# Kernel tuning notes

Hardware: AMD Instinct MI355X
Metric: run time of the kernel (lower is better)

## Reference

```python
import jax, jax.numpy as jnp
from jax import lax
import numpy as np

B, S, D = 64, 512, 256
VOCAB, NC = 50000, 10
N_STEPS = 10  # ode_step=11 points -> 10 intervals, h=0.1
BN_EPS = 1e-5


def setup_inputs() -> dict:
    key = jax.random.key(0)
    ks = jax.random.split(key, 16)
    inp = {}
    inp['input_ids'] = jax.random.randint(ks[0], (B, S), 0, VOCAB)
    inp['emb'] = jax.random.normal(ks[1], (VOCAB, D), dtype=jnp.float32)
    inp['W_ode'] = 0.1 * jax.random.normal(ks[2], (D, D), dtype=jnp.float32)  # init std=0.1
    inp['b_ode'] = jnp.zeros((D,), dtype=jnp.float32)
    for i, kk in enumerate([3, 4, 5]):
        fan_in = D * kk
        inp[f'w{kk}'] = jax.random.normal(ks[3 + 3 * i], (128, D, kk), jnp.float32) / np.sqrt(fan_in)
        inp[f'b{kk}'] = jax.random.normal(ks[4 + 3 * i], (128,), jnp.float32) * 0.01
        inp[f'g{kk}'] = jnp.ones((128,), jnp.float32)
        inp[f'be{kk}'] = jnp.zeros((128,), jnp.float32)
    inp['wc'] = jax.random.normal(ks[12], (NC, D + 3 * 128), jnp.float32) / np.sqrt(D + 3 * 128)
    inp['bc'] = jnp.zeros((NC,), jnp.float32)
    return inp


def _forward(input_ids, emb, W_ode, b_ode, w3, b3, g3, be3, w4, b4, g4, be4,
             w5, b5, g5, be5, wc, bc):
    x = emb[input_ids]                      # (B,S,D)
    # --- Neural ODE branch: linear RHS f(z) = z W^T + b, RK4 fixed-step on [0,1] ---
    z0 = x.reshape(-1, D)                   # (B*S, D)
    h = jnp.float32(1.0 / N_STEPS)

    def f(z):
        return z @ W_ode.T + b_ode

    def step(z, _):
        k1 = f(z)
        k2 = f(z + 0.5 * h * k1)
        k3 = f(z + 0.5 * h * k2)
        k4 = f(z + h * k3)
        return z + (h / 6.0) * (k1 + 2 * k2 + 2 * k3 + k4), None

    z, _ = lax.scan(step, z0, None, length=N_STEPS)
    node_pooled = z.reshape(B, S, D).max(axis=1)   # global max over seq -> (B,D)

    # --- TextCNN branches on raw embeddings ---
    cin = jnp.transpose(x, (0, 2, 1))       # (B,D,S)
    inv_std = jnp.float32(1.0 / np.sqrt(1.0 + BN_EPS))  # BN eval: mean=0, var=1

    def branch(w, b, g, be):
        c = lax.conv_general_dilated(cin, w, (1,), 'VALID',
                                     dimension_numbers=('NCH', 'OIH', 'NCH'))
        c = c + b[None, :, None]
        c = g[None, :, None] * (c * inv_std) + be[None, :, None]
        c = jax.nn.relu(c)
        return c.max(axis=2)                # (B,128)

    p3 = branch(w3, b3, g3, be3)
    p4 = branch(w4, b4, g4, be4)
    p5 = branch(w5, b5, g5, be5)

    feats = jnp.concatenate([node_pooled, p3, p4, p5], axis=1)  # (B,640)
    return feats @ wc.T + bc                # (B,NC); dropout is identity in eval


def reference(input_ids, emb, W_ode, b_ode, w3, b3, g3, be3, w4, b4, g4, be4,
              w5, b5, g5, be5, wc, bc):
    return _forward(input_ids, emb, W_ode, b_ode, w3, b3, g3, be3,
                    w4, b4, g4, be4, w5, b5, g5, be5, wc, bc)
```

## Files before the change

kernel.cpp:

```cpp
#include <hip/hip_runtime.h>


typedef short bf16x8 __attribute__((ext_vector_type(8)));
typedef float f32x4 __attribute__((ext_vector_type(4)));

__device__ __forceinline__ unsigned short f2bf(float f) {
  unsigned u = __float_as_uint(f);
  u += 0x7FFFu + ((u >> 16) & 1u);
  return (unsigned short)(u >> 16);
}

__device__ __forceinline__ float dotcol64(const float* __restrict__ xrow,
                                          const float* __restrict__ Y, int c) {
  float a0 = 0.f, a1 = 0.f, a2 = 0.f, a3 = 0.f;
#pragma unroll 1
  for (int w = 0; w < 4; ++w) {
    float bv[64];
#pragma unroll
    for (int v = 0; v < 64; ++v) bv[v] = Y[(w * 64 + v) * 256 + c];
#pragma unroll
    for (int v = 0; v < 64; v += 4) {
      a0 = fmaf(xrow[w * 64 + v + 0], bv[v + 0], a0);
      a1 = fmaf(xrow[w * 64 + v + 1], bv[v + 1], a1);
      a2 = fmaf(xrow[w * 64 + v + 2], bv[v + 2], a2);
      a3 = fmaf(xrow[w * 64 + v + 3], bv[v + 3], a3);
    }
  }
  return (a0 + a1) + (a2 + a3);
}

__global__ __launch_bounds__(256) void k_prep1(
    const float* __restrict__ W, const float* __restrict__ bode,
    const float* __restrict__ w3c, const float* __restrict__ w4c, const float* __restrict__ w5c,
    float* __restrict__ Bm, float* __restrict__ c1,
    unsigned short* __restrict__ slab, unsigned* __restrict__ featbuf) {
  __shared__ float r1[256], r2[256], r3[256], red[4];
  const int tid = threadIdx.x, blk = blockIdx.x;
  if (blk < 256) {
    const int i = blk;
    r1[tid] = W[i * 256 + tid];
    __syncthreads();
    const float v2 = dotcol64(r1, W, tid);
    r2[tid] = v2;
    __syncthreads();
    const float v3 = dotcol64(r2, W, tid);
    r3[tid] = v3;
    __syncthreads();
    const float v4 = dotcol64(r3, W, tid);
    const float w1 = r1[tid];
    Bm[i * 256 + tid] = 0.1f * w1 + 0.005f * v2
                      + (0.001f / 6.f) * v3 + (0.0001f / 24.f) * v4;
    const float q = 0.05f * w1 + (0.01f / 6.f) * v2 + (0.001f / 24.f) * v3;
    float val = bode[tid] * q;
#pragma unroll
    for (int off = 32; off > 0; off >>= 1) val += __shfl_down(val, off);
    if ((tid & 63) == 0) red[tid >> 6] = val;
    __syncthreads();
    if (tid == 0) c1[i] = 0.1f * (bode[i] + ((red[0] + red[1]) + (red[2] + red[3])));
  } else {
    const int base = (blk - 256) * 256 + tid;
#pragma unroll
    for (int u = 0; u < 4; ++u) {
      int e = base + u * 98304;
      int s = e >> 15, r = e & 32767;
      int o = r >> 8, kd = r & 255;
      const float* w; int k, j;
      if (s < 3)      { w = w3c; k = 3; j = s; }
      else if (s < 7) { w = w4c; k = 4; j = s - 3; }
      else            { w = w5c; k = 5; j = s - 7; }
      float val = w[(o * 256 + kd) * k + j];
      int kc = kd >> 5, quad = (kd >> 3) & 3, q8 = kd & 7;
      slab[s * 32768 + ((kc * 4 + quad) * 128 + o) * 8 + q8] = f2bf(val);
    }
    if (base < 64 * 640) featbuf[base] = 0u;
  }
}

__global__ __launch_bounds__(256) void k_prep2a(
    const float* __restrict__ Bm, const float* __restrict__ c1v,
    float* __restrict__ Dm, float* __restrict__ c1b) {
  __shared__ float r1[256], c1s[256], red[4];
  const int tid = threadIdx.x, i = blockIdx.x;
  r1[tid] = Bm[i * 256 + tid];
  c1s[tid] = c1v[tid];
  __syncthreads();
  const float v2 = dotcol64(r1, Bm, tid);
  Dm[i * 256 + tid] = 2.f * r1[tid] + v2;
  float pd = r1[tid] * c1s[tid];
#pragma unroll
  for (int off = 32; off > 0; off >>= 1) pd += __shfl_down(pd, off);
  if ((tid & 63) == 0) red[tid >> 6] = pd;
  __syncthreads();
  if (tid == 0) c1b[i] = 2.f * c1s[i] + ((red[0] + red[1]) + (red[2] + red[3]));
}

__global__ __launch_bounds__(256) void k_prep2b(
    const float* __restrict__ Dm, const float* __restrict__ c1bv,
    float* __restrict__ c10, unsigned short* __restrict__ slab) {
  __shared__ float curs[256], cbs[256], red[4];
  const int tid = threadIdx.x, i = blockIdx.x;
  const float coefN[6] = {1.f, 5.f, 10.f, 10.f, 5.f, 1.f};
  const float coefC[5] = {5.f, 10.f, 10.f, 5.f, 1.f};
  float v = Dm[i * 256 + tid];
  curs[tid] = v;
  cbs[tid] = c1bv[tid];
  __syncthreads();
  float n10 = ((i == tid) ? 1.f : 0.f) + coefN[1] * v;
  float pd = v * cbs[tid];
#pragma unroll
  for (int off = 32; off > 0; off >>= 1) pd += __shfl_down(pd, off);
  if ((tid & 63) == 0) red[tid >> 6] = pd;
  __syncthreads();
  float ct = coefC[0] * cbs[i] + coefC[1] * ((red[0] + red[1]) + (red[2] + red[3]));

#pragma unroll 1
  for (int k = 2; k <= 5; ++k) {
    v = dotcol64(curs, Dm, tid);
    __syncthreads();
    curs[tid] = v;
    n10 = fmaf(coefN[k], v, n10);
    float pdk = v * cbs[tid];
#pragma unroll
    for (int off = 32; off > 0; off >>= 1) pdk += __shfl_down(pdk, off);
    if ((tid & 63) == 0) red[tid >> 6] = pdk;
    __syncthreads();
    if (k <= 4) ct = fmaf(coefC[k], (red[0] + red[1]) + (red[2] + red[3]), ct);
  }

  {
    const int o = i, kd = tid;
    const int kc = kd >> 5, quad = (kd >> 3) & 3, q8 = kd & 7;
    slab[(12 + (o >> 7)) * 32768 + ((kc * 4 + quad) * 128 + (o & 127)) * 8 + q8] = f2bf(n10);
  }
  if (tid == 0) c10[i] = ct;
}


__global__ __launch_bounds__(256, 2) void k_main(
    const int* __restrict__ ids, const float* __restrict__ emb,
    const unsigned short* __restrict__ slab, const float* __restrict__ ctot,
    const float* __restrict__ b3, const float* __restrict__ g3, const float* __restrict__ be3,
    const float* __restrict__ b4, const float* __restrict__ g4, const float* __restrict__ be4,
    const float* __restrict__ b5, const float* __restrict__ g5, const float* __restrict__ be5,
    unsigned* __restrict__ featbuf) {
  __shared__ alignas(16) unsigned short Xt[68 * 264];
  __shared__ int ids_s[68];
  const int tid = threadIdx.x;
  const int blk = blockIdx.x;
  const int b = blk >> 3;
  const int t0 = (blk & 7) * 64;
  const int lane = tid & 63;
  const int wave = tid >> 6;
  const int m15 = lane & 15;
  const int quad = lane >> 4;

  if (tid < 68) {
    int t = t0 + tid;
    ids_s[tid] = (t < 512) ? ids[b * 512 + t] : -1;
  }
  __syncthreads();

  const unsigned short* fb0 = slab + ((size_t)quad * 128 + wave * 2 * 16 + m15) * 8;
  bf16x8 fA[4], fB[4], fC[4], fD[4];
#define LDFRAG(DST, EN)                                                         \
  {                                                                             \
    const unsigned short* p_ = fb0 + (EN) * 8192;                               \
    DST[0] = *(const bf16x8*)(p_);                                              \
    DST[1] = *(const bf16x8*)(p_ + 128);                                        \
    DST[2] = *(const bf16x8*)(p_ + 4096);                                       \
    DST[3] = *(const bf16x8*)(p_ + 4096 + 128);                                 \
  }
  LDFRAG(fA, 0) LDFRAG(fB, 1) LDFRAG(fC, 2) LDFRAG(fD, 3)

  for (int i = tid; i < 68 * 64; i += 256) {
    int row = i >> 6, s4 = i & 63;
    uint2 v = make_uint2(0u, 0u);
    int id = ids_s[row];
    if (id >= 0) {
      const float4 f = *(const float4*)(emb + (size_t)id * 256 + s4 * 4);
      v.x = (unsigned)f2bf(f.x) | ((unsigned)f2bf(f.y) << 16);
      v.y = (unsigned)f2bf(f.z) | ((unsigned)f2bf(f.w) << 16);
    }
    *(uint2*)&Xt[row * 264 + s4 * 4] = v;
  }
  __syncthreads();

  f32x4 acc[4][2];
#pragma unroll
  for (int mt = 0; mt < 4; ++mt)
#pragma unroll
    for (int nt = 0; nt < 2; ++nt) acc[mt][nt] = (f32x4){0.f, 0.f, 0.f, 0.f};

#define ENTRY(KCQ, FR)                                                          \
  {                                                                             \
    _Pragma("unroll")                                                           \
    for (int kc2 = 0; kc2 < 2; ++kc2) {                                         \
      const int kd0 = ((KCQ) * 2 + kc2) * 32 + quad * 8;                        \
      bf16x8 af[4];                                                             \
      _Pragma("unroll")                                                         \
      for (int mt = 0; mt < 4; ++mt)                                            \
        af[mt] = *(const bf16x8*)&Xt[(shift + mt * 16 + m15) * 264 + kd0];      \
      _Pragma("unroll")                                                         \
      for (int mt = 0; mt < 4; ++mt) {                                          \
        acc[mt][0] = __builtin_amdgcn_mfma_f32_16x16x32_bf16(af[mt], FR[kc2 * 2 + 0], acc[mt][0], 0, 0, 0); \
        acc[mt][1] = __builtin_amdgcn_mfma_f32_16x16x32_bf16(af[mt], FR[kc2 * 2 + 1], acc[mt][1], 0, 0, 0); \
      }                                                                         \
    }                                                                           \
  }

  for (int eq = 0; eq < 14; ++eq) {
    const int shift = (eq < 3) ? eq : (eq < 7) ? (eq - 3) : (eq < 12) ? (eq - 7) : 0;

    ENTRY(0, fA) if (eq < 13) LDFRAG(fA, (eq + 1) * 4 + 0)
    ENTRY(1, fB) if (eq < 13) LDFRAG(fB, (eq + 1) * 4 + 1)
    ENTRY(2, fC) if (eq < 13) LDFRAG(fC, (eq + 1) * 4 + 2)
    ENTRY(3, fD) if (eq < 13) LDFRAG(fD, (eq + 1) * 4 + 3)

    const int g = (eq == 2) ? 0 : (eq == 6) ? 1 : (eq == 11) ? 2
                : (eq == 12) ? 3 : (eq == 13) ? 4 : -1;
    if (g >= 0) {
      if (g < 3) {
        const int kk = g + 3;
        const float* bb  = (g == 0) ? b3 : (g == 1) ? b4 : b5;
        const float* gg  = (g == 0) ? g3 : (g == 1) ? g4 : g5;
        const float* bbe = (g == 0) ? be3 : (g == 1) ? be4 : be5;
        const int off = 256 + g * 128;
        const int tmax = 512 - kk;
#pragma unroll
        for (int nt = 0; nt < 2; ++nt) {
          const int n = (wave * 2 + nt) * 16 + m15;
          const float sc = gg[n] * 0.9999950000375f;
          const float sh = fmaf(sc, bb[n], bbe[n]);
          float mx = 0.f;
#pragma unroll
          for (int mt = 0; mt < 4; ++mt)
#pragma unroll
            for (int r = 0; r < 4; ++r) {
              const int t = t0 + mt * 16 + quad * 4 + r;
              const float v = fmaf(sc, acc[mt][nt][r], sh);
              if (t <= tmax) mx = fmaxf(mx, v);
            }
          mx = fmaxf(mx, __shfl_xor(mx, 16));
          mx = fmaxf(mx, __shfl_xor(mx, 32));
          if (quad == 0) atomicMax(&featbuf[b * 640 + off + n], __float_as_uint(mx));
        }
      } else {
        const int base = (g == 3) ? 0 : 128;
#pragma unroll
        for (int nt = 0; nt < 2; ++nt) {
          const int n = (wave * 2 + nt) * 16 + m15;
          const float ct = ctot[base + n];
          float mx = -3.4e38f;
#pragma unroll
          for (int mt = 0; mt < 4; ++mt)
#pragma unroll
            for (int r = 0; r < 4; ++r)
              mx = fmaxf(mx, acc[mt][nt][r] + ct);
          mx = fmaxf(mx, __shfl_xor(mx, 16));
          mx = fmaxf(mx, __shfl_xor(mx, 32));
          if (quad == 0) {
            unsigned bits = __float_as_uint(mx);
            unsigned key = (bits & 0x80000000u) ? ~bits : (bits | 0x80000000u);
            atomicMax(&featbuf[b * 640 + base + n], key);
          }
        }
      }
#pragma unroll
      for (int mt = 0; mt < 4; ++mt)
#pragma unroll
        for (int nt = 0; nt < 2; ++nt) acc[mt][nt] = (f32x4){0.f, 0.f, 0.f, 0.f};
    }
  }
#undef ENTRY
#undef LDFRAG
}

__global__ void k_fin(const unsigned* __restrict__ featbuf, const float* __restrict__ wc,
                      const float* __restrict__ bc, float* __restrict__ out) {
  int b = blockIdx.x, lane = threadIdx.x;
  float p[10];
#pragma unroll
  for (int c = 0; c < 10; ++c) p[c] = 0.f;
  for (int f = lane; f < 640; f += 64) {
    unsigned u = featbuf[b * 640 + f];
    float v;
    if (f < 256) v = (u & 0x80000000u) ? __uint_as_float(u ^ 0x80000000u) : __uint_as_float(~u);
    else v = __uint_as_float(u);
#pragma unroll
    for (int c = 0; c < 10; ++c) p[c] = fmaf(v, wc[c * 640 + f], p[c]);
  }
#pragma unroll
  for (int c = 0; c < 10; ++c) {
    float s = p[c];
#pragma unroll
    for (int off = 32; off > 0; off >>= 1) s += __shfl_down(s, off);
    if (lane == 0) out[b * 10 + c] = s + bc[c];
  }
}

extern "C" void kernel_launch(void* const* d_in, const int* in_sizes, int n_in,
                              void* d_out, int out_size, void* d_ws, size_t ws_size,
                              hipStream_t stream) {
  (void)in_sizes; (void)n_in; (void)out_size; (void)ws_size;
  const int*   ids  = (const int*)d_in[0];
  const float* emb  = (const float*)d_in[1];
  const float* W    = (const float*)d_in[2];
  const float* bode = (const float*)d_in[3];
  const float* w3   = (const float*)d_in[4];
  const float* b3   = (const float*)d_in[5];
  const float* g3   = (const float*)d_in[6];
  const float* be3  = (const float*)d_in[7];
  const float* w4   = (const float*)d_in[8];
  const float* b4   = (const float*)d_in[9];
  const float* g4   = (const float*)d_in[10];
  const float* be4  = (const float*)d_in[11];
  const float* w5   = (const float*)d_in[12];
  const float* b5   = (const float*)d_in[13];
  const float* g5   = (const float*)d_in[14];
  const float* be5  = (const float*)d_in[15];
  const float* wc   = (const float*)d_in[16];
  const float* bc   = (const float*)d_in[17];
  float* out = (float*)d_out;

  float* wsf = (float*)d_ws;
  float* Bm  = wsf;
  float* Dm  = wsf + 65536;
  float* c1  = wsf + 131072;
  float* c1b = wsf + 131328;
  float* c10 = wsf + 131584;
  unsigned short* slab = (unsigned short*)(wsf + 131840);
  unsigned* featbuf = (unsigned*)(wsf + 361216);

  hipLaunchKernelGGL(k_prep1, dim3(640), dim3(256), 0, stream,
                     W, bode, w3, w4, w5, Bm, c1, slab, featbuf);
  hipLaunchKernelGGL(k_prep2a, dim3(256), dim3(256), 0, stream, Bm, c1, Dm, c1b);
  hipLaunchKernelGGL(k_prep2b, dim3(256), dim3(256), 0, stream, Dm, c1b, c10, slab);
  hipLaunchKernelGGL(k_main, dim3(512), dim3(256), 0, stream,
                     ids, emb, slab, c10,
                     b3, g3, be3, b4, g4, be4, b5, g5, be5, featbuf);
  hipLaunchKernelGGL(k_fin, dim3(64), dim3(64), 0, stream, featbuf, wc, bc, out);
}
```

Before: 195.7 us.

## Halve k_main time tile to 32, double grid, double-buffer weight fragments

Each k_main block now covers 32 sequence positions instead of 64, so the grid grows to 1024 blocks and launch bounds rise to 4 blocks per CU. Weight-fragment prefetch drops from four buffers to two, so the loop now runs 28 steps over two slab entries each. MFMA sections are wrapped in s_setprio. The goal is more occupancy and less register and LDS use per block. The cost is that every slab fragment is re-read by twice as many blocks, with more global and L2 traffic and twice as many atomicMax updates.

```diff
diff --git a/kernel.cpp b/kernel.cpp
--- a/kernel.cpp
+++ b/kernel.cpp
@@ -136,43 +136,30 @@
 }
 
 
-__global__ __launch_bounds__(256, 2) void k_main(
+__global__ __launch_bounds__(256, 4) void k_main(
     const int* __restrict__ ids, const float* __restrict__ emb,
     const unsigned short* __restrict__ slab, const float* __restrict__ ctot,
     const float* __restrict__ b3, const float* __restrict__ g3, const float* __restrict__ be3,
     const float* __restrict__ b4, const float* __restrict__ g4, const float* __restrict__ be4,
     const float* __restrict__ b5, const float* __restrict__ g5, const float* __restrict__ be5,
     unsigned* __restrict__ featbuf) {
-  __shared__ alignas(16) unsigned short Xt[68 * 264];
-  __shared__ int ids_s[68];
+  __shared__ alignas(16) unsigned short Xt[36 * 264];
+  __shared__ int ids_s[36];
   const int tid = threadIdx.x;
   const int blk = blockIdx.x;
-  const int b = blk >> 3;
-  const int t0 = (blk & 7) * 64;
+  const int b = blk & 63;
+  const int t0 = (blk >> 6) * 32;
   const int lane = tid & 63;
   const int wave = tid >> 6;
   const int m15 = lane & 15;
   const int quad = lane >> 4;
 
-  if (tid < 68) {
+  if (tid < 36) {
     int t = t0 + tid;
     ids_s[tid] = (t < 512) ? ids[b * 512 + t] : -1;
   }
   __syncthreads();
-
-  const unsigned short* fb0 = slab + ((size_t)quad * 128 + wave * 2 * 16 + m15) * 8;
-  bf16x8 fA[4], fB[4], fC[4], fD[4];
-#define LDFRAG(DST, EN)                                                         \
-  {                                                                             \
-    const unsigned short* p_ = fb0 + (EN) * 8192;                               \
-    DST[0] = *(const bf16x8*)(p_);                                              \
-    DST[1] = *(const bf16x8*)(p_ + 128);                                        \
-    DST[2] = *(const bf16x8*)(p_ + 4096);                                       \
-    DST[3] = *(const bf16x8*)(p_ + 4096 + 128);                                 \
-  }
-  LDFRAG(fA, 0) LDFRAG(fB, 1) LDFRAG(fC, 2) LDFRAG(fD, 3)
-
-  for (int i = tid; i < 68 * 64; i += 256) {
+  for (int i = tid; i < 36 * 64; i += 256) {
     int row = i >> 6, s4 = i & 63;
     uint2 v = make_uint2(0u, 0u);
     int id = ids_s[row];
@@ -185,39 +172,66 @@
   }
   __syncthreads();
 
-  f32x4 acc[4][2];
-#pragma unroll
-  for (int mt = 0; mt < 4; ++mt)
+  const unsigned short* fb0 = slab + ((size_t)quad * 128 + (wave * 2 + 0) * 16 + m15) * 8;
+  const unsigned short* fb1 = fb0 + 128;
+
+  bf16x8 fA[4], fB[4];
+#pragma unroll
+  for (int q = 0; q < 4; ++q) {
+    fA[q] = *(const bf16x8*)(((q & 1) ? fb1 : fb0) + (q >> 1) * 4096);
+    fB[q] = *(const bf16x8*)(((q & 1) ? fb1 : fb0) + 8192 + (q >> 1) * 4096);
+  }
+
+  f32x4 acc[2][2];
+#pragma unroll
+  for (int mt = 0; mt < 2; ++mt)
 #pragma unroll
     for (int nt = 0; nt < 2; ++nt) acc[mt][nt] = (f32x4){0.f, 0.f, 0.f, 0.f};
 
 #define ENTRY(KCQ, FR)                                                          \
   {                                                                             \
+    __builtin_amdgcn_s_setprio(1);                                              \
     _Pragma("unroll")                                                           \
     for (int kc2 = 0; kc2 < 2; ++kc2) {                                         \
       const int kd0 = ((KCQ) * 2 + kc2) * 32 + quad * 8;                        \
-      bf16x8 af[4];                                                             \
+      bf16x8 af[2];                                                             \
       _Pragma("unroll")                                                         \
-      for (int mt = 0; mt < 4; ++mt)                                            \
+      for (int mt = 0; mt < 2; ++mt)                                            \
         af[mt] = *(const bf16x8*)&Xt[(shift + mt * 16 + m15) * 264 + kd0];      \
       _Pragma("unroll")                                                         \
-      for (int mt = 0; mt < 4; ++mt) {                                          \
+      for (int mt = 0; mt < 2; ++mt) {                                          \
         acc[mt][0] = __builtin_amdgcn_mfma_f32_16x16x32_bf16(af[mt], FR[kc2 * 2 + 0], acc[mt][0], 0, 0, 0); \
         acc[mt][1] = __builtin_amdgcn_mfma_f32_16x16x32_bf16(af[mt], FR[kc2 * 2 + 1], acc[mt][1], 0, 0, 0); \
       }                                                                         \
     }                                                                           \
-  }
-
-  for (int eq = 0; eq < 14; ++eq) {
-    const int shift = (eq < 3) ? eq : (eq < 7) ? (eq - 3) : (eq < 12) ? (eq - 7) : 0;
-
-    ENTRY(0, fA) if (eq < 13) LDFRAG(fA, (eq + 1) * 4 + 0)
-    ENTRY(1, fB) if (eq < 13) LDFRAG(fB, (eq + 1) * 4 + 1)
-    ENTRY(2, fC) if (eq < 13) LDFRAG(fC, (eq + 1) * 4 + 2)
-    ENTRY(3, fD) if (eq < 13) LDFRAG(fD, (eq + 1) * 4 + 3)
-
-    const int g = (eq == 2) ? 0 : (eq == 6) ? 1 : (eq == 11) ? 2
-                : (eq == 12) ? 3 : (eq == 13) ? 4 : -1;
+    __builtin_amdgcn_s_setprio(0);                                              \
+  }
+
+  for (int ep = 0; ep < 28; ++ep) {
+    const int e0 = ep * 2;
+    const int slice = e0 >> 2;
+    const int shift = (slice < 3) ? slice
+                    : (slice < 7) ? (slice - 3)
+                    : (slice < 12) ? (slice - 7) : 0;
+    const int kcq0 = e0 & 3;
+
+    ENTRY(kcq0, fA);
+    if (ep < 27) {
+      const int eo = (e0 + 2) * 8192;
+#pragma unroll
+      for (int q = 0; q < 4; ++q)
+        fA[q] = *(const bf16x8*)(((q & 1) ? fb1 : fb0) + eo + (q >> 1) * 4096);
+    }
+    ENTRY(kcq0 + 1, fB);
+    if (ep < 27) {
+      const int eo = (e0 + 3) * 8192;
+#pragma unroll
+      for (int q = 0; q < 4; ++q)
+        fB[q] = *(const bf16x8*)(((q & 1) ? fb1 : fb0) + eo + (q >> 1) * 4096);
+    }
+
+    const int g = (ep == 5) ? 0 : (ep == 13) ? 1 : (ep == 23) ? 2
+                : (ep == 25) ? 3 : (ep == 27) ? 4 : -1;
     if (g >= 0) {
       if (g < 3) {
         const int kk = g + 3;
@@ -233,7 +247,7 @@
           const float sh = fmaf(sc, bb[n], bbe[n]);
           float mx = 0.f;
 #pragma unroll
-          for (int mt = 0; mt < 4; ++mt)
+          for (int mt = 0; mt < 2; ++mt)
 #pragma unroll
             for (int r = 0; r < 4; ++r) {
               const int t = t0 + mt * 16 + quad * 4 + r;
@@ -252,7 +266,7 @@
           const float ct = ctot[base + n];
           float mx = -3.4e38f;
 #pragma unroll
-          for (int mt = 0; mt < 4; ++mt)
+          for (int mt = 0; mt < 2; ++mt)
 #pragma unroll
             for (int r = 0; r < 4; ++r)
               mx = fmaxf(mx, acc[mt][nt][r] + ct);
@@ -266,13 +280,12 @@
         }
       }
 #pragma unroll
-      for (int mt = 0; mt < 4; ++mt)
+      for (int mt = 0; mt < 2; ++mt)
 #pragma unroll
         for (int nt = 0; nt < 2; ++nt) acc[mt][nt] = (f32x4){0.f, 0.f, 0.f, 0.f};
     }
   }
 #undef ENTRY
-#undef LDFRAG
 }
 
 __global__ void k_fin(const unsigned* __restrict__ featbuf, const float* __restrict__ wc,
@@ -335,7 +348,7 @@
                      W, bode, w3, w4, w5, Bm, c1, slab, featbuf);
   hipLaunchKernelGGL(k_prep2a, dim3(256), dim3(256), 0, stream, Bm, c1, Dm, c1b);
   hipLaunchKernelGGL(k_prep2b, dim3(256), dim3(256), 0, stream, Dm, c1b, c10, slab);
-  hipLaunchKernelGGL(k_main, dim3(512), dim3(256), 0, stream,
+  hipLaunchKernelGGL(k_main, dim3(1024), dim3(256), 0, stream,
                      ids, emb, slab, c10,
                      b3, g3, be3, b4, g4, be4, b5, g5, be5, featbuf);
   hipLaunchKernelGGL(k_fin, dim3(64), dim3(64), 0, stream, featbuf, wc, bc, out);
```

Result: slower. 202.7 us (+3.6%).

## Double block sizes: split-K prep matvecs and 8-wave MFMA tiling in main

Applied to the files above, without the earlier changes.

The prep kernels move to 512 threads. Each column dot product is split across two thread halves over K and the two partials are combined through shared memory, which shortens the serial matrix-power chains. The main kernel uses 8 waves per block instead of 4. Each wave now owns one 16-row M tile and four N tiles, with fragments double-buffered in two register sets instead of four. The aim is more latency hiding and parallelism, at the cost of extra barriers and fewer accumulators per wave, and with a changed register-pressure balance under launch_bounds(512,4).

```diff
diff --git a/kernel.cpp b/kernel.cpp
--- a/kernel.cpp
+++ b/kernel.cpp
@@ -10,55 +10,63 @@
   return (unsigned short)(u >> 16);
 }
 
-__device__ __forceinline__ float dotcol64(const float* __restrict__ xrow,
-                                          const float* __restrict__ Y, int c) {
+__device__ __forceinline__ float rpass512(const float* __restrict__ src,
+                                          const float* __restrict__ Y,
+                                          float* __restrict__ part,
+                                          int c, int g, int t) {
   float a0 = 0.f, a1 = 0.f, a2 = 0.f, a3 = 0.f;
 #pragma unroll 1
-  for (int w = 0; w < 4; ++w) {
+  for (int w2 = 0; w2 < 2; ++w2) {
+    const int k0 = g * 128 + w2 * 64;
     float bv[64];
 #pragma unroll
-    for (int v = 0; v < 64; ++v) bv[v] = Y[(w * 64 + v) * 256 + c];
+    for (int v = 0; v < 64; ++v) bv[v] = Y[(size_t)(k0 + v) * 256 + c];
 #pragma unroll
     for (int v = 0; v < 64; v += 4) {
-      a0 = fmaf(xrow[w * 64 + v + 0], bv[v + 0], a0);
-      a1 = fmaf(xrow[w * 64 + v + 1], bv[v + 1], a1);
-      a2 = fmaf(xrow[w * 64 + v + 2], bv[v + 2], a2);
-      a3 = fmaf(xrow[w * 64 + v + 3], bv[v + 3], a3);
-    }
-  }
-  return (a0 + a1) + (a2 + a3);
-}
-
-__global__ __launch_bounds__(256) void k_prep1(
+      a0 = fmaf(src[k0 + v + 0], bv[v + 0], a0);
+      a1 = fmaf(src[k0 + v + 1], bv[v + 1], a1);
+      a2 = fmaf(src[k0 + v + 2], bv[v + 2], a2);
+      a3 = fmaf(src[k0 + v + 3], bv[v + 3], a3);
+    }
+  }
+  part[t] = (a0 + a1) + (a2 + a3);
+  __syncthreads();
+  return (t < 256) ? (part[t] + part[t + 256]) : 0.f;
+}
+
+__global__ __launch_bounds__(512) void k_prep1(
     const float* __restrict__ W, const float* __restrict__ bode,
     const float* __restrict__ w3c, const float* __restrict__ w4c, const float* __restrict__ w5c,
     float* __restrict__ Bm, float* __restrict__ c1,
     unsigned short* __restrict__ slab, unsigned* __restrict__ featbuf) {
-  __shared__ float r1[256], r2[256], r3[256], red[4];
-  const int tid = threadIdx.x, blk = blockIdx.x;
+  __shared__ float part[512], r1[256], r2[256], r3[256], red[4];
+  const int t = threadIdx.x, blk = blockIdx.x;
+  const int c = t & 255, g = t >> 8;
   if (blk < 256) {
     const int i = blk;
-    r1[tid] = W[i * 256 + tid];
-    __syncthreads();
-    const float v2 = dotcol64(r1, W, tid);
-    r2[tid] = v2;
-    __syncthreads();
-    const float v3 = dotcol64(r2, W, tid);
-    r3[tid] = v3;
-    __syncthreads();
-    const float v4 = dotcol64(r3, W, tid);
-    const float w1 = r1[tid];
-    Bm[i * 256 + tid] = 0.1f * w1 + 0.005f * v2
+    if (t < 256) r1[t] = W[i * 256 + t];
+    __syncthreads();
+    const float v2 = rpass512(r1, W, part, c, g, t);
+    if (t < 256) r2[t] = v2;
+    __syncthreads();
+    const float v3 = rpass512(r2, W, part, c, g, t);
+    if (t < 256) r3[t] = v3;
+    __syncthreads();
+    const float v4 = rpass512(r3, W, part, c, g, t);
+    if (t < 256) {
+      const float w1 = r1[t];
+      Bm[i * 256 + t] = 0.1f * w1 + 0.005f * v2
                       + (0.001f / 6.f) * v3 + (0.0001f / 24.f) * v4;
-    const float q = 0.05f * w1 + (0.01f / 6.f) * v2 + (0.001f / 24.f) * v3;
-    float val = bode[tid] * q;
-#pragma unroll
-    for (int off = 32; off > 0; off >>= 1) val += __shfl_down(val, off);
-    if ((tid & 63) == 0) red[tid >> 6] = val;
-    __syncthreads();
-    if (tid == 0) c1[i] = 0.1f * (bode[i] + ((red[0] + red[1]) + (red[2] + red[3])));
+      const float q = 0.05f * w1 + (0.01f / 6.f) * v2 + (0.001f / 24.f) * v3;
+      float val = bode[t] * q;
+#pragma unroll
+      for (int off = 32; off > 0; off >>= 1) val += __shfl_down(val, off);
+      if ((t & 63) == 0) red[t >> 6] = val;
+    }
+    __syncthreads();
+    if (t == 0) c1[i] = 0.1f * (bode[i] + ((red[0] + red[1]) + (red[2] + red[3])));
   } else {
-    const int base = (blk - 256) * 256 + tid;
+    const int base = (blk - 256) * 512 + t;
 #pragma unroll
     for (int u = 0; u < 4; ++u) {
       int e = base + u * 98304;
@@ -76,67 +84,77 @@
   }
 }
 
-__global__ __launch_bounds__(256) void k_prep2a(
+__global__ __launch_bounds__(512) void k_prep2a(
     const float* __restrict__ Bm, const float* __restrict__ c1v,
     float* __restrict__ Dm, float* __restrict__ c1b) {
-  __shared__ float r1[256], c1s[256], red[4];
-  const int tid = threadIdx.x, i = blockIdx.x;
-  r1[tid] = Bm[i * 256 + tid];
-  c1s[tid] = c1v[tid];
-  __syncthreads();
-  const float v2 = dotcol64(r1, Bm, tid);
-  Dm[i * 256 + tid] = 2.f * r1[tid] + v2;
-  float pd = r1[tid] * c1s[tid];
-#pragma unroll
-  for (int off = 32; off > 0; off >>= 1) pd += __shfl_down(pd, off);
-  if ((tid & 63) == 0) red[tid >> 6] = pd;
-  __syncthreads();
-  if (tid == 0) c1b[i] = 2.f * c1s[i] + ((red[0] + red[1]) + (red[2] + red[3]));
-}
-
-__global__ __launch_bounds__(256) void k_prep2b(
+  __shared__ float part[512], r1[256], c1s[256], red[4];
+  const int t = threadIdx.x, i = blockIdx.x;
+  const int c = t & 255, g = t >> 8;
+  if (t < 256) { r1[t] = Bm[i * 256 + t]; c1s[t] = c1v[t]; }
+  __syncthreads();
+  const float v2 = rpass512(r1, Bm, part, c, g, t);
+  if (t < 256) {
+    Dm[i * 256 + t] = 2.f * r1[t] + v2;
+    float pd = r1[t] * c1s[t];
+#pragma unroll
+    for (int off = 32; off > 0; off >>= 1) pd += __shfl_down(pd, off);
+    if ((t & 63) == 0) red[t >> 6] = pd;
+  }
+  __syncthreads();
+  if (t == 0) c1b[i] = 2.f * c1s[i] + ((red[0] + red[1]) + (red[2] + red[3]));
+}
+
+__global__ __launch_bounds__(512) void k_prep2b(
     const float* __restrict__ Dm, const float* __restrict__ c1bv,
     float* __restrict__ c10, unsigned short* __restrict__ slab) {
-  __shared__ float curs[256], cbs[256], red[4];
-  const int tid = threadIdx.x, i = blockIdx.x;
+  __shared__ float part[512], curs[256], cbs[256], red[4];
+  const int t = threadIdx.x, i = blockIdx.x;
+  const int c = t & 255, g = t >> 8;
   const float coefN[6] = {1.f, 5.f, 10.f, 10.f, 5.f, 1.f};
   const float coefC[5] = {5.f, 10.f, 10.f, 5.f, 1.f};
-  float v = Dm[i * 256 + tid];
-  curs[tid] = v;
-  cbs[tid] = c1bv[tid];
-  __syncthreads();
-  float n10 = ((i == tid) ? 1.f : 0.f) + coefN[1] * v;
-  float pd = v * cbs[tid];
-#pragma unroll
-  for (int off = 32; off > 0; off >>= 1) pd += __shfl_down(pd, off);
-  if ((tid & 63) == 0) red[tid >> 6] = pd;
-  __syncthreads();
-  float ct = coefC[0] * cbs[i] + coefC[1] * ((red[0] + red[1]) + (red[2] + red[3]));
+  float v = 0.f, n10 = 0.f, ct = 0.f;
+  if (t < 256) {
+    v = Dm[i * 256 + t];
+    curs[t] = v;
+    cbs[t] = c1bv[t];
+  }
+  __syncthreads();
+  if (t < 256) {
+    n10 = ((i == t) ? 1.f : 0.f) + coefN[1] * v;
+    float pd = v * cbs[t];
+#pragma unroll
+    for (int off = 32; off > 0; off >>= 1) pd += __shfl_down(pd, off);
+    if ((t & 63) == 0) red[t >> 6] = pd;
+  }
+  __syncthreads();
+  if (t < 256) ct = coefC[0] * cbs[i] + coefC[1] * ((red[0] + red[1]) + (red[2] + red[3]));
 
 #pragma unroll 1
   for (int k = 2; k <= 5; ++k) {
-    v = dotcol64(curs, Dm, tid);
-    __syncthreads();
-    curs[tid] = v;
-    n10 = fmaf(coefN[k], v, n10);
-    float pdk = v * cbs[tid];
-#pragma unroll
-    for (int off = 32; off > 0; off >>= 1) pdk += __shfl_down(pdk, off);
-    if ((tid & 63) == 0) red[tid >> 6] = pdk;
-    __syncthreads();
-    if (k <= 4) ct = fmaf(coefC[k], (red[0] + red[1]) + (red[2] + red[3]), ct);
-  }
-
-  {
-    const int o = i, kd = tid;
+    v = rpass512(curs, Dm, part, c, g, t);
+    if (t < 256) {
+      curs[t] = v;
+      n10 = fmaf(coefN[k], v, n10);
+      float pdk = v * cbs[t];
+#pragma unroll
+      for (int off = 32; off > 0; off >>= 1) pdk += __shfl_down(pdk, off);
+      if ((t & 63) == 0) red[t >> 6] = pdk;
+    }
+    __syncthreads();
+    if (t < 256 && k <= 4)
+      ct = fmaf(coefC[k], (red[0] + red[1]) + (red[2] + red[3]), ct);
+  }
+
+  if (t < 256) {
+    const int o = i, kd = t;
     const int kc = kd >> 5, quad = (kd >> 3) & 3, q8 = kd & 7;
     slab[(12 + (o >> 7)) * 32768 + ((kc * 4 + quad) * 128 + (o & 127)) * 8 + q8] = f2bf(n10);
   }
-  if (tid == 0) c10[i] = ct;
-}
-
-
-__global__ __launch_bounds__(256, 2) void k_main(
+  if (t == 0) c10[i] = ct;
+}
+
+
+__global__ __launch_bounds__(512, 4) void k_main(
     const int* __restrict__ ids, const float* __restrict__ emb,
     const unsigned short* __restrict__ slab, const float* __restrict__ ctot,
     const float* __restrict__ b3, const float* __restrict__ g3, const float* __restrict__ be3,
@@ -153,6 +171,8 @@
   const int wave = tid >> 6;
   const int m15 = lane & 15;
   const int quad = lane >> 4;
+  const int mtw = wave & 3;
+  const int ntq = wave >> 2;
 
   if (tid < 68) {
     int t = t0 + tid;
@@ -160,19 +180,18 @@
   }
   __syncthreads();
 
-  const unsigned short* fb0 = slab + ((size_t)quad * 128 + wave * 2 * 16 + m15) * 8;
-  bf16x8 fA[4], fB[4], fC[4], fD[4];
+  const unsigned short* fb0 = slab + (size_t)quad * 1024 + ntq * 512 + m15 * 8;
+  bf16x8 fA[8], fB[8];
 #define LDFRAG(DST, EN)                                                         \
   {                                                                             \
-    const unsigned short* p_ = fb0 + (EN) * 8192;                               \
-    DST[0] = *(const bf16x8*)(p_);                                              \
-    DST[1] = *(const bf16x8*)(p_ + 128);                                        \
-    DST[2] = *(const bf16x8*)(p_ + 4096);                                       \
-    DST[3] = *(const bf16x8*)(p_ + 4096 + 128);                                 \
-  }
-  LDFRAG(fA, 0) LDFRAG(fB, 1) LDFRAG(fC, 2) LDFRAG(fD, 3)
-
-  for (int i = tid; i < 68 * 64; i += 256) {
+    const unsigned short* p_ = fb0 + (size_t)(EN) * 8192;                       \
+    _Pragma("unroll")                                                           \
+    for (int q = 0; q < 8; ++q)                                                 \
+      DST[q] = *(const bf16x8*)(p_ + (q >> 2) * 4096 + (q & 3) * 128);          \
+  }
+  LDFRAG(fA, 0) LDFRAG(fB, 1)
+
+  for (int i = tid; i < 68 * 64; i += 512) {
     int row = i >> 6, s4 = i & 63;
     uint2 v = make_uint2(0u, 0u);
     int id = ids_s[row];
@@ -185,39 +204,37 @@
   }
   __syncthreads();
 
-  f32x4 acc[4][2];
-#pragma unroll
-  for (int mt = 0; mt < 4; ++mt)
-#pragma unroll
-    for (int nt = 0; nt < 2; ++nt) acc[mt][nt] = (f32x4){0.f, 0.f, 0.f, 0.f};
+  f32x4 acc[4];
+#pragma unroll
+  for (int ntl = 0; ntl < 4; ++ntl) acc[ntl] = (f32x4){0.f, 0.f, 0.f, 0.f};
 
 #define ENTRY(KCQ, FR)                                                          \
   {                                                                             \
     _Pragma("unroll")                                                           \
     for (int kc2 = 0; kc2 < 2; ++kc2) {                                         \
       const int kd0 = ((KCQ) * 2 + kc2) * 32 + quad * 8;                        \
-      bf16x8 af[4];                                                             \
+      const bf16x8 af = *(const bf16x8*)&Xt[(shift + mtw * 16 + m15) * 264 + kd0]; \
       _Pragma("unroll")                                                         \
-      for (int mt = 0; mt < 4; ++mt)                                            \
-        af[mt] = *(const bf16x8*)&Xt[(shift + mt * 16 + m15) * 264 + kd0];      \
-      _Pragma("unroll")                                                         \
-      for (int mt = 0; mt < 4; ++mt) {                                          \
-        acc[mt][0] = __builtin_amdgcn_mfma_f32_16x16x32_bf16(af[mt], FR[kc2 * 2 + 0], acc[mt][0], 0, 0, 0); \
-        acc[mt][1] = __builtin_amdgcn_mfma_f32_16x16x32_bf16(af[mt], FR[kc2 * 2 + 1], acc[mt][1], 0, 0, 0); \
-      }                                                                         \
+      for (int ntl = 0; ntl < 4; ++ntl)                                         \
+        acc[ntl] = __builtin_amdgcn_mfma_f32_16x16x32_bf16(af, FR[kc2 * 4 + ntl], acc[ntl], 0, 0, 0); \
     }                                                                           \
   }
 
-  for (int eq = 0; eq < 14; ++eq) {
-    const int shift = (eq < 3) ? eq : (eq < 7) ? (eq - 3) : (eq < 12) ? (eq - 7) : 0;
-
-    ENTRY(0, fA) if (eq < 13) LDFRAG(fA, (eq + 1) * 4 + 0)
-    ENTRY(1, fB) if (eq < 13) LDFRAG(fB, (eq + 1) * 4 + 1)
-    ENTRY(2, fC) if (eq < 13) LDFRAG(fC, (eq + 1) * 4 + 2)
-    ENTRY(3, fD) if (eq < 13) LDFRAG(fD, (eq + 1) * 4 + 3)
-
-    const int g = (eq == 2) ? 0 : (eq == 6) ? 1 : (eq == 11) ? 2
-                : (eq == 12) ? 3 : (eq == 13) ? 4 : -1;
+  for (int ep = 0; ep < 28; ++ep) {
+    const int e0 = ep * 2;
+    const int slice = e0 >> 2;
+    const int shift = (slice < 3) ? slice
+                    : (slice < 7) ? (slice - 3)
+                    : (slice < 12) ? (slice - 7) : 0;
+    const int kcq0 = e0 & 3;
+
+    ENTRY(kcq0, fA);
+    if (ep < 27) LDFRAG(fA, e0 + 2)
+    ENTRY(kcq0 + 1, fB);
+    if (ep < 27) LDFRAG(fB, e0 + 3)
+
+    const int g = (ep == 5) ? 0 : (ep == 13) ? 1 : (ep == 23) ? 2
+                : (ep == 25) ? 3 : (ep == 27) ? 4 : -1;
     if (g >= 0) {
       if (g < 3) {
         const int kk = g + 3;
@@ -227,19 +244,17 @@
         const int off = 256 + g * 128;
         const int tmax = 512 - kk;
 #pragma unroll
-        for (int nt = 0; nt < 2; ++nt) {
-          const int n = (wave * 2 + nt) * 16 + m15;
+        for (int ntl = 0; ntl < 4; ++ntl) {
+          const int n = (ntq * 4 + ntl) * 16 + m15;
           const float sc = gg[n] * 0.9999950000375f;
           const float sh = fmaf(sc, bb[n], bbe[n]);
           float mx = 0.f;
 #pragma unroll
-          for (int mt = 0; mt < 4; ++mt)
-#pragma unroll
-            for (int r = 0; r < 4; ++r) {
-              const int t = t0 + mt * 16 + quad * 4 + r;
-              const float v = fmaf(sc, acc[mt][nt][r], sh);
-              if (t <= tmax) mx = fmaxf(mx, v);
-            }
+          for (int r = 0; r < 4; ++r) {
+            const int t = t0 + mtw * 16 + quad * 4 + r;
+            const float v = fmaf(sc, acc[ntl][r], sh);
+            if (t <= tmax) mx = fmaxf(mx, v);
+          }
           mx = fmaxf(mx, __shfl_xor(mx, 16));
           mx = fmaxf(mx, __shfl_xor(mx, 32));
           if (quad == 0) atomicMax(&featbuf[b * 640 + off + n], __float_as_uint(mx));
@@ -247,15 +262,13 @@
       } else {
         const int base = (g == 3) ? 0 : 128;
 #pragma unroll
-        for (int nt = 0; nt < 2; ++nt) {
-          const int n = (wave * 2 + nt) * 16 + m15;
+        for (int ntl = 0; ntl < 4; ++ntl) {
+          const int n = (ntq * 4 + ntl) * 16 + m15;
           const float ct = ctot[base + n];
           float mx = -3.4e38f;
 #pragma unroll
-          for (int mt = 0; mt < 4; ++mt)
-#pragma unroll
-            for (int r = 0; r < 4; ++r)
-              mx = fmaxf(mx, acc[mt][nt][r] + ct);
+          for (int r = 0; r < 4; ++r)
+            mx = fmaxf(mx, acc[ntl][r] + ct);
           mx = fmaxf(mx, __shfl_xor(mx, 16));
           mx = fmaxf(mx, __shfl_xor(mx, 32));
           if (quad == 0) {
@@ -266,9 +279,7 @@
         }
       }
 #pragma unroll
-      for (int mt = 0; mt < 4; ++mt)
-#pragma unroll
-        for (int nt = 0; nt < 2; ++nt) acc[mt][nt] = (f32x4){0.f, 0.f, 0.f, 0.f};
+      for (int ntl = 0; ntl < 4; ++ntl) acc[ntl] = (f32x4){0.f, 0.f, 0.f, 0.f};
     }
   }
 #undef ENTRY
@@ -331,11 +342,11 @@
   unsigned short* slab = (unsigned short*)(wsf + 131840);
   unsigned* featbuf = (unsigned*)(wsf + 361216);
 
-  hipLaunchKernelGGL(k_prep1, dim3(640), dim3(256), 0, stream,
+  hipLaunchKernelGGL(k_prep1, dim3(448), dim3(512), 0, stream,
                      W, bode, w3, w4, w5, Bm, c1, slab, featbuf);
-  hipLaunchKernelGGL(k_prep2a, dim3(256), dim3(256), 0, stream, Bm, c1, Dm, c1b);
-  hipLaunchKernelGGL(k_prep2b, dim3(256), dim3(256), 0, stream, Dm, c1b, c10, slab);
-  hipLaunchKernelGGL(k_main, dim3(512), dim3(256), 0, stream,
+  hipLaunchKernelGGL(k_prep2a, dim3(256), dim3(512), 0, stream, Bm, c1, Dm, c1b);
+  hipLaunchKernelGGL(k_prep2b, dim3(256), dim3(512), 0, stream, Dm, c1b, c10, slab);
+  hipLaunchKernelGGL(k_main, dim3(512), dim3(512), 0, stream,
                      ids, emb, slab, c10,
                      b3, g3, be3, b4, g4, be4, b5, g5, be5, featbuf);
   hipLaunchKernelGGL(k_fin, dim3(64), dim3(64), 0, stream, featbuf, wc, bc, out);
```

Result: slower. 219.6 us (+12.2%).
